# Kernel optimization log

Hardware: AMD Instinct MI355X
Metric: run time of the kernel (lower is better)

Reference implementation:

```python
import jax, jax.numpy as jnp
import numpy as np

N_HEADS = 8
INPUT_DIM = 256
KEY_DIM = 64
VALUE_DIM = 64
BATCH = 16
GRAPH = 1024
NEG_INF = -1e30  # finite stand-in for -inf: safe through softmax under jit/grad


def setup_inputs() -> dict:
    key = jax.random.key(0)
    k_h, k_m, k_q, k_k, k_v = jax.random.split(key, 5)
    h = jax.random.normal(k_h, (BATCH, GRAPH, INPUT_DIM), dtype=jnp.float32)
    # anti-adjacency matrix: 1 = disallowed edge, 0 = allowed
    mask = jax.random.randint(k_m, (GRAPH, GRAPH), 0, 2, dtype=jnp.int32)
    W_Q = jax.random.normal(k_q, (N_HEADS, INPUT_DIM, KEY_DIM), dtype=jnp.float32)
    W_K = jax.random.normal(k_k, (N_HEADS, INPUT_DIM, KEY_DIM), dtype=jnp.float32)
    W_V = jax.random.normal(k_v, (N_HEADS, INPUT_DIM, VALUE_DIM), dtype=jnp.float32)
    return {"h": h, "mask": mask, "W_Q": W_Q, "W_K": W_K, "W_V": W_V}


def reference(h, mask, W_Q, W_K, W_V):
    # h: [b, g, i]; W_*: [h, i, d]
    scale = 1.0 / jnp.sqrt(jnp.asarray(W_Q.shape[-1], h.dtype))
    q = jnp.einsum('bgi,hik->bhgk', h, W_Q)  # [b,h,g,dk]
    k = jnp.einsum('bgi,hik->bhgk', h, W_K)  # [b,h,g,dk]
    v = jnp.einsum('bgi,hiv->bhgv', h, W_V)  # [b,h,g,dv]
    compat = scale * jnp.einsum('bhqk,bhmk->bhqm', q, k)  # [b,h,g,g]
    allowed = (mask == 0)  # [g,g], broadcasts over batch/heads
    compat = jnp.where(allowed, compat, NEG_INF)
    attention = jax.nn.softmax(compat, axis=-1)
    # original zeroes attention at masked positions after softmax
    attention = jnp.where(allowed, attention, 0.0)
    h_p = jnp.einsum('bhqm,bhmv->bhqv', attention, v)  # [b,h,g,dv]
    return h_p
```

## Files before the change

### kernel.cpp

```cpp
#include <hip/hip_runtime.h>
#include <math.h>

typedef __bf16 bf16x8 __attribute__((ext_vector_type(8)));
typedef float  f32x4  __attribute__((ext_vector_type(4)));

#define NEGB   (-1.4426950408889634e30f)
#define SCALE2 (0.18033688011112042f)

template <int N> struct ic { static constexpr int value = N; };

static __device__ __forceinline__ f32x4 mfma16(bf16x8 a, bf16x8 b, f32x4 c) {
    return __builtin_amdgcn_mfma_f32_16x16x32_bf16(a, b, c, 0, 0, 0);
}

static __device__ __forceinline__ void load_lds16(const void* g, void* l) {
    __builtin_amdgcn_global_load_lds(
        (const __attribute__((address_space(1))) unsigned int*)g,
        (__attribute__((address_space(3))) unsigned int*)l, 16, 0, 0);
}

template <int CTRL>
static __device__ __forceinline__ float dppf(float x) {
    int xi = __builtin_bit_cast(int, x);
    int r = __builtin_amdgcn_update_dpp(xi, xi, CTRL, 0xf, 0xf, false);
    return __builtin_bit_cast(float, r);
}
static __device__ __forceinline__ float rowmax16(float x) {
    x = fmaxf(x, dppf<0x128>(x));
    x = fmaxf(x, dppf<0x124>(x));
    x = fmaxf(x, dppf<0x122>(x));
    x = fmaxf(x, dppf<0x121>(x));
    return x;
}
static __device__ __forceinline__ float rowsum16(float x) {
    x += dppf<0x128>(x);
    x += dppf<0x124>(x);
    x += dppf<0x122>(x);
    x += dppf<0x121>(x);
    return x;
}

#define RAW_BARRIER() asm volatile("s_waitcnt lgkmcnt(0)\n\ts_barrier" ::: "memory")

__global__ void prep_kernel(const int* __restrict__ mask,
                            const float* __restrict__ Wq, const float* __restrict__ Wk,
                            const float* __restrict__ Wv,
                            unsigned long long* __restrict__ mbits,
                            __bf16* __restrict__ Whi_t, __bf16* __restrict__ Wlo_t)
{
    const int tid = threadIdx.x;
    if (blockIdx.x < 1024) {
        const int row = blockIdx.x, wave = tid >> 6, lane = tid & 63;
        #pragma unroll
        for (int i = 0; i < 4; ++i) {
            int word = wave * 4 + i;
            int m = mask[row * 1024 + word * 64 + lane];
            unsigned long long b = __ballot(m != 0);
            if (lane == 0) mbits[row * 16 + word] = b;
        }
    } else {
        int idx = (blockIdx.x - 1024) * 256 + tid;
        int lane = idx & 63, t = (idx >> 6) & 3, kc = (idx >> 8) & 7;
        int head = (idx >> 11) & 7, mat = idx >> 14;
        int quad = lane >> 4, ln = lane & 15;
        const float* W = (mat == 0 ? Wq : (mat == 1 ? Wk : Wv)) + head * 16384;
        bf16x8 hi, lo;
        #pragma unroll
        for (int j = 0; j < 8; ++j) {
            float w = W[(kc * 32 + quad * 8 + j) * 64 + t * 16 + ln];
            __bf16 hh = (__bf16)w;
            hi[j] = hh;
            lo[j] = (__bf16)(w - (float)hh);
        }
        *(bf16x8*)(Whi_t + (size_t)idx * 8) = hi;
        *(bf16x8*)(Wlo_t + (size_t)idx * 8) = lo;
    }
}

__global__ __launch_bounds__(256, 2) void projkv_kernel(
    const float* __restrict__ X,
    const __bf16* __restrict__ Whi_t, const __bf16* __restrict__ Wlo_t,
    unsigned char* __restrict__ khi_g, unsigned char* __restrict__ klo_g,
    unsigned char* __restrict__ vT_g)
{
    const int head = blockIdx.x, rt = blockIdx.y;
    const int tid = threadIdx.x, wave = tid >> 6, lane = tid & 63;
    const int quad = lane >> 4, ln = lane & 15;

    __shared__ __align__(16) unsigned char SL[24576];

    const float* xr = X + ((size_t)(rt * 64 + wave * 16 + ln)) * 256;
    bf16x8 ahi[8], alo[8];
    #pragma unroll
    for (int kc = 0; kc < 8; ++kc) {
        f32x4 xa = *(const f32x4*)(xr + kc * 32 + quad * 8);
        f32x4 xb = *(const f32x4*)(xr + kc * 32 + quad * 8 + 4);
        #pragma unroll
        for (int j = 0; j < 4; ++j) {
            __bf16 h0 = (__bf16)xa[j]; ahi[kc][j] = h0; alo[kc][j] = (__bf16)(xa[j] - (float)h0);
            __bf16 h1 = (__bf16)xb[j]; ahi[kc][4 + j] = h1; alo[kc][4 + j] = (__bf16)(xb[j] - (float)h1);
        }
    }

    const __bf16* WhiK = Whi_t + ((size_t)(8 + head) * 2048) * 8;
    const __bf16* WloK = Wlo_t + ((size_t)(8 + head) * 2048) * 8;
    const __bf16* WhiV = Whi_t + ((size_t)(16 + head) * 2048) * 8;

    f32x4 kacc[4], vacc[4];
    #pragma unroll
    for (int t = 0; t < 4; ++t) { kacc[t] = (f32x4){0.f,0.f,0.f,0.f}; vacc[t] = kacc[t]; }

    #pragma unroll
    for (int kc = 0; kc < 8; ++kc) {
        #pragma unroll
        for (int t = 0; t < 4; ++t) {
            size_t fo = (size_t)((kc * 4 + t) * 64 + lane) * 8;
            bf16x8 bhiK = *(const bf16x8*)(WhiK + fo);
            bf16x8 bloK = *(const bf16x8*)(WloK + fo);
            bf16x8 bhiV = *(const bf16x8*)(WhiV + fo);
            kacc[t] = mfma16(ahi[kc], bhiK, kacc[t]);
            kacc[t] = mfma16(alo[kc], bhiK, kacc[t]);
            kacc[t] = mfma16(ahi[kc], bloK, kacc[t]);
            vacc[t] = mfma16(ahi[kc], bhiV, vacc[t]);
        }
    }

    #pragma unroll
    for (int t = 0; t < 4; ++t) {
        #pragma unroll
        for (int r = 0; r < 4; ++r) {
            {
                float val = kacc[t][r];
                __bf16 hh = (__bf16)val;
                __bf16 ll = (__bf16)(val - (float)hh);
                int row = wave * 16 + quad * 4 + r;
                int lc = t * 2 + (ln >> 3);
                int sc = lc ^ (row & 7);
                int off = (row * 8 + sc) * 16 + (ln & 7) * 2;
                *(__bf16*)(SL + off) = hh;
                *(__bf16*)(SL + 8192 + off) = ll;
            }
            {
                int dvrow = t * 16 + ln;
                int m = wave * 16 + quad * 4 + r;
                int lc = m >> 3;
                int sc = lc ^ (ln & 7);
                int off = (dvrow * 8 + sc) * 16 + (m & 7) * 2;
                *(__bf16*)(SL + 16384 + off) = (__bf16)vacc[t][r];
            }
        }
    }
    __syncthreads();

    const int bh = (rt >> 4) * 8 + head;
    const int mt = rt & 15;
    const size_t tb = (size_t)(bh * 16 + mt) * 8192;
    #pragma unroll
    for (int i = 0; i < 2; ++i) {
        int c = (i * 256 + tid) * 16;
        *(uint4*)(khi_g + tb + c) = *(const uint4*)(SL + c);
        *(uint4*)(klo_g + tb + c) = *(const uint4*)(SL + 8192 + c);
        *(uint4*)(vT_g  + tb + c) = *(const uint4*)(SL + 16384 + c);
    }
}

__global__ __launch_bounds__(256, 2) void attn_kernel(
    const float* __restrict__ X,
    const __bf16* __restrict__ Whi_t, const __bf16* __restrict__ Wlo_t,
    const unsigned char* __restrict__ khi_g, const unsigned char* __restrict__ klo_g,
    const unsigned char* __restrict__ vT_g, const unsigned long long* __restrict__ mbits,
    float* __restrict__ out)
{
    const int qt = blockIdx.y;
    const int bh = blockIdx.x;
    const int b = bh >> 3, head = bh & 7;
    const int tid = threadIdx.x, wave = tid >> 6, lane = tid & 63;
    const int quad = lane >> 4, ln = lane & 15;

    __shared__ __align__(16) unsigned char lds[49152];

    f32x4 qacc[2][4];
    #pragma unroll
    for (int rg = 0; rg < 2; ++rg)
        #pragma unroll
        for (int t = 0; t < 4; ++t) qacc[rg][t] = (f32x4){0.f, 0.f, 0.f, 0.f};

    const __bf16* WhiQ = Whi_t + (size_t)head * 2048 * 8;
    const __bf16* WloQ = Wlo_t + (size_t)head * 2048 * 8;

    #pragma unroll
    for (int kc = 0; kc < 8; ++kc) {
        bf16x8 ahi[2], alo[2];
        #pragma unroll
        for (int rg = 0; rg < 2; ++rg) {
            const float* xr = X + ((size_t)b * 1024 + qt * 128 + wave * 32 + rg * 16 + ln) * 256;
            f32x4 xa = *(const f32x4*)(xr + kc * 32 + quad * 8);
            f32x4 xb = *(const f32x4*)(xr + kc * 32 + quad * 8 + 4);
            #pragma unroll
            for (int j = 0; j < 4; ++j) {
                __bf16 h0 = (__bf16)xa[j]; ahi[rg][j] = h0; alo[rg][j] = (__bf16)(xa[j] - (float)h0);
                __bf16 h1 = (__bf16)xb[j]; ahi[rg][4 + j] = h1; alo[rg][4 + j] = (__bf16)(xb[j] - (float)h1);
            }
        }
        #pragma unroll
        for (int t = 0; t < 4; ++t) {
            size_t fo = (size_t)((kc * 4 + t) * 64 + lane) * 8;
            bf16x8 bhi = *(const bf16x8*)(WhiQ + fo);
            bf16x8 blo = *(const bf16x8*)(WloQ + fo);
            #pragma unroll
            for (int rg = 0; rg < 2; ++rg) {
                qacc[rg][t] = mfma16(ahi[rg], bhi, qacc[rg][t]);
                qacc[rg][t] = mfma16(alo[rg], bhi, qacc[rg][t]);
                qacc[rg][t] = mfma16(ahi[rg], blo, qacc[rg][t]);
            }
        }
    }

    #pragma unroll
    for (int rg = 0; rg < 2; ++rg)
        #pragma unroll
        for (int t = 0; t < 4; ++t) {
            qacc[rg][t] *= SCALE2;
            #pragma unroll
            for (int r = 0; r < 4; ++r)
                *(float*)(lds + wave * 8704 + (rg * 16 + quad * 4 + r) * 272 + (t * 16 + ln) * 4) =
                    qacc[rg][t][r];
        }
    bf16x8 qhi[2][2], qlo[2][2];
    #pragma unroll
    for (int rg = 0; rg < 2; ++rg)
        #pragma unroll
        for (int c = 0; c < 2; ++c) {
            f32x4 a0 = *(const f32x4*)(lds + wave * 8704 + (rg * 16 + ln) * 272 + c * 128 + quad * 32);
            f32x4 a1 = *(const f32x4*)(lds + wave * 8704 + (rg * 16 + ln) * 272 + c * 128 + quad * 32 + 16);
            #pragma unroll
            for (int j = 0; j < 4; ++j) {
                __bf16 h0 = (__bf16)a0[j]; qhi[rg][c][j] = h0; qlo[rg][c][j] = (__bf16)(a0[j] - (float)h0);
                __bf16 h1 = (__bf16)a1[j]; qhi[rg][c][4 + j] = h1; qlo[rg][c][4 + j] = (__bf16)(a1[j] - (float)h1);
            }
        }
    __syncthreads();

    int addrA[4][2], addrP[2];
    #pragma unroll
    for (int t = 0; t < 4; ++t)
        #pragma unroll
        for (int c = 0; c < 2; ++c)
            addrA[t][c] = (t * 16 + ln) * 128 + (((c * 4 + quad) ^ (ln & 7)) << 4);
    #pragma unroll
    for (int c = 0; c < 2; ++c)
        addrP[c] = ln * 128 + (((c * 4 + quad) ^ (ln & 7)) << 4);

    f32x4 o[2][4];
    float mrow[2][4], lrow[2][4];
    #pragma unroll
    for (int rg = 0; rg < 2; ++rg)
        #pragma unroll
        for (int t = 0; t < 4; ++t) {
            o[rg][t] = (f32x4){0.f, 0.f, 0.f, 0.f};
            mrow[rg][t] = -INFINITY; lrow[rg][t] = 0.f;
        }

    const int qrow0 = qt * 128 + wave * 32 + quad * 4;

    auto stage = [&](int mt, int bufb) {
        const unsigned char* kb = khi_g + (size_t)(bh * 16 + mt) * 8192;
        const unsigned char* lb = klo_g + (size_t)(bh * 16 + mt) * 8192;
        const unsigned char* vb = vT_g + (size_t)(bh * 16 + mt) * 8192;
        #pragma unroll
        for (int j = 0; j < 2; ++j) {
            int ch = j * 256 + wave * 64;
            load_lds16(kb + (size_t)(ch + lane) * 16, lds + bufb + ch * 16);
            load_lds16(lb + (size_t)(ch + lane) * 16, lds + bufb + 8192 + ch * 16);
            load_lds16(vb + (size_t)(ch + lane) * 16, lds + bufb + 16384 + ch * 16);
        }
    };

    auto step = [&](auto bofc, int mt) {
        constexpr int BOFF = decltype(bofc)::value;
        if (mt < 15) stage(mt + 1, 24576 - BOFF);

        uint2 wm[2][4];
        #pragma unroll
        for (int rg = 0; rg < 2; ++rg)
            #pragma unroll
            for (int r = 0; r < 4; ++r)
                wm[rg][r] = *(const uint2*)((const unsigned char*)mbits +
                                            ((size_t)(qrow0 + rg * 16 + r) * 16 + mt) * 8);

        f32x4 s[2][4];
        #pragma unroll
        for (int rg = 0; rg < 2; ++rg)
            #pragma unroll
            for (int t = 0; t < 4; ++t) s[rg][t] = (f32x4){0.f, 0.f, 0.f, 0.f};
        #pragma unroll
        for (int t = 0; t < 4; ++t)
            #pragma unroll
            for (int c = 0; c < 2; ++c) {
                bf16x8 khi = *(const bf16x8*)(lds + BOFF + addrA[t][c]);
                bf16x8 klo = *(const bf16x8*)(lds + BOFF + 8192 + addrA[t][c]);
                #pragma unroll
                for (int rg = 0; rg < 2; ++rg) {
                    s[rg][t] = mfma16(qhi[rg][c], khi, s[rg][t]);
                    s[rg][t] = mfma16(qlo[rg][c], khi, s[rg][t]);
                    s[rg][t] = mfma16(qhi[rg][c], klo, s[rg][t]);
                }
            }

        RAW_BARRIER();

        #pragma unroll
        for (int rg = 0; rg < 2; ++rg) {
            float pw[4][4], alpha[4];
            #pragma unroll
            for (int r = 0; r < 4; ++r) {
                float sv[4];
                #pragma unroll
                for (int t = 0; t < 4; ++t) {
                    unsigned bits = (t & 2) ? wm[rg][r].y : wm[rg][r].x;
                    float bit = (float)((bits >> ((t & 1) * 16 + ln)) & 1u);
                    sv[t] = fmaf(bit, NEGB, s[rg][t][r]);
                }
                float tm = fmaxf(fmaxf(sv[0], sv[1]), fmaxf(sv[2], sv[3]));
                tm = rowmax16(tm);
                float mn = fmaxf(mrow[rg][r], tm);
                float a = __builtin_amdgcn_exp2f(mrow[rg][r] - mn);
                float rs = 0.f;
                #pragma unroll
                for (int t = 0; t < 4; ++t) {
                    float p = __builtin_amdgcn_exp2f(sv[t] - mn);
                    pw[r][t] = p; rs += p;
                }
                rs = rowsum16(rs);
                lrow[rg][r] = lrow[rg][r] * a + rs;
                mrow[rg][r] = mn;
                alpha[r] = a;
            }
            #pragma unroll
            for (int t = 0; t < 4; ++t)
                #pragma unroll
                for (int r = 0; r < 4; ++r) o[rg][t][r] *= alpha[r];
            #pragma unroll
            for (int t = 0; t < 4; ++t) {
                int lc16 = t * 32 + ((ln >> 3) << 4);
                #pragma unroll
                for (int r = 0; r < 4; ++r) {
                    int row = quad * 4 + r;
                    int addr = BOFF + wave * 4096 + rg * 2048 + row * 128 +
                               (lc16 ^ ((row & 7) << 4)) + ((ln & 7) << 1);
                    *(__bf16*)(lds + addr) = (__bf16)pw[r][t];
                }
            }
        }
        asm volatile("s_waitcnt lgkmcnt(0)" ::: "memory");

        #pragma unroll
        for (int c = 0; c < 2; ++c) {
            bf16x8 pa[2];
            #pragma unroll
            for (int rg = 0; rg < 2; ++rg)
                pa[rg] = *(const bf16x8*)(lds + BOFF + wave * 4096 + rg * 2048 + addrP[c]);
            #pragma unroll
            for (int t = 0; t < 4; ++t) {
                bf16x8 vb = *(const bf16x8*)(lds + BOFF + 16384 + addrA[t][c]);
                #pragma unroll
                for (int rg = 0; rg < 2; ++rg) o[rg][t] = mfma16(pa[rg], vb, o[rg][t]);
            }
        }
        __syncthreads();
    };

    stage(0, 0);
    __syncthreads();
    for (int mp = 0; mp < 8; ++mp) {
        step(ic<0>{}, 2 * mp);
        step(ic<24576>{}, 2 * mp + 1);
    }

    float* ob = out + (size_t)bh * 65536;
    #pragma unroll
    for (int rg = 0; rg < 2; ++rg)
        #pragma unroll
        for (int r = 0; r < 4; ++r) {
            float inv = 1.0f / lrow[rg][r];
            #pragma unroll
            for (int t = 0; t < 4; ++t)
                ob[(size_t)(qrow0 + rg * 16 + r) * 64 + t * 16 + ln] = o[rg][t][r] * inv;
        }
}

extern "C" void kernel_launch(void* const* d_in, const int* in_sizes, int n_in,
                              void* d_out, int out_size, void* d_ws, size_t ws_size,
                              hipStream_t stream) {
    const float* h    = (const float*)d_in[0];
    const int*   mask = (const int*)d_in[1];
    const float* Wq   = (const float*)d_in[2];
    const float* Wk   = (const float*)d_in[3];
    const float* Wv   = (const float*)d_in[4];
    float* out = (float*)d_out;

    unsigned char* ws = (unsigned char*)d_ws;
    unsigned char* khi_g = ws;
    unsigned char* klo_g = ws + 16777216;
    unsigned char* vT_g  = ws + 33554432;
    __bf16* Whi_t = (__bf16*)(ws + 50331648);
    __bf16* Wlo_t = (__bf16*)(ws + 51118080);
    unsigned long long* mbits = (unsigned long long*)(ws + 51904512);

    prep_kernel<<<1216, 256, 0, stream>>>(mask, Wq, Wk, Wv, mbits, Whi_t, Wlo_t);
    projkv_kernel<<<dim3(8, 256), 256, 0, stream>>>(h, Whi_t, Wlo_t, khi_g, klo_g, vT_g);
    attn_kernel<<<dim3(128, 8), 256, 0, stream>>>(h, Whi_t, Wlo_t, khi_g, klo_g, vT_g, mbits, out);
}
```

Measured before the change: 248.4 us.

## Load K/V MFMA fragments directly from global memory and reuse X rows across heads

The attention kernel drops the LDS double-buffered staging of K/V tiles and their block barriers. projkv now writes K and V^T pre-arranged in MFMA fragment order, so each lane reads its bf16x8 operands straight from global memory and only the per-wave P matrix goes through LDS. projkv also handles four heads per block, so X is loaded and split into hi/lo once for four heads instead of once per head. The cost is global/L2 latency exposed inside the inner loop with no explicit prefetch, and fewer, longer projkv blocks.

Measured after the change: 299.9 us. 20.7% more time.

```diff
diff --git a/kernel.cpp b/kernel.cpp
--- a/kernel.cpp
+++ b/kernel.cpp
@@ -7,16 +7,8 @@
 #define NEGB   (-1.4426950408889634e30f)
 #define SCALE2 (0.18033688011112042f)
 
-template <int N> struct ic { static constexpr int value = N; };
-
 static __device__ __forceinline__ f32x4 mfma16(bf16x8 a, bf16x8 b, f32x4 c) {
     return __builtin_amdgcn_mfma_f32_16x16x32_bf16(a, b, c, 0, 0, 0);
-}
-
-static __device__ __forceinline__ void load_lds16(const void* g, void* l) {
-    __builtin_amdgcn_global_load_lds(
-        (const __attribute__((address_space(1))) unsigned int*)g,
-        (__attribute__((address_space(3))) unsigned int*)l, 16, 0, 0);
 }
 
 template <int CTRL>
@@ -39,8 +31,6 @@
     x += dppf<0x121>(x);
     return x;
 }
-
-#define RAW_BARRIER() asm volatile("s_waitcnt lgkmcnt(0)\n\ts_barrier" ::: "memory")
 
 __global__ void prep_kernel(const int* __restrict__ mask,
                             const float* __restrict__ Wq, const float* __restrict__ Wk,
@@ -83,7 +73,8 @@
     unsigned char* __restrict__ khi_g, unsigned char* __restrict__ klo_g,
     unsigned char* __restrict__ vT_g)
 {
-    const int head = blockIdx.x, rt = blockIdx.y;
+    const int hh = blockIdx.x;
+    const int rt = blockIdx.y;
     const int tid = threadIdx.x, wave = tid >> 6, lane = tid & 63;
     const int quad = lane >> 4, ln = lane & 15;
 
@@ -102,65 +93,67 @@
         }
     }
 
-    const __bf16* WhiK = Whi_t + ((size_t)(8 + head) * 2048) * 8;
-    const __bf16* WloK = Wlo_t + ((size_t)(8 + head) * 2048) * 8;
-    const __bf16* WhiV = Whi_t + ((size_t)(16 + head) * 2048) * 8;
-
-    f32x4 kacc[4], vacc[4];
-    #pragma unroll
-    for (int t = 0; t < 4; ++t) { kacc[t] = (f32x4){0.f,0.f,0.f,0.f}; vacc[t] = kacc[t]; }
-
-    #pragma unroll
-    for (int kc = 0; kc < 8; ++kc) {
-        #pragma unroll
-        for (int t = 0; t < 4; ++t) {
-            size_t fo = (size_t)((kc * 4 + t) * 64 + lane) * 8;
-            bf16x8 bhiK = *(const bf16x8*)(WhiK + fo);
-            bf16x8 bloK = *(const bf16x8*)(WloK + fo);
-            bf16x8 bhiV = *(const bf16x8*)(WhiV + fo);
-            kacc[t] = mfma16(ahi[kc], bhiK, kacc[t]);
-            kacc[t] = mfma16(alo[kc], bhiK, kacc[t]);
-            kacc[t] = mfma16(ahi[kc], bloK, kacc[t]);
-            vacc[t] = mfma16(ahi[kc], bhiV, vacc[t]);
-        }
-    }
-
-    #pragma unroll
-    for (int t = 0; t < 4; ++t) {
-        #pragma unroll
-        for (int r = 0; r < 4; ++r) {
-            {
-                float val = kacc[t][r];
-                __bf16 hh = (__bf16)val;
-                __bf16 ll = (__bf16)(val - (float)hh);
-                int row = wave * 16 + quad * 4 + r;
-                int lc = t * 2 + (ln >> 3);
-                int sc = lc ^ (row & 7);
-                int off = (row * 8 + sc) * 16 + (ln & 7) * 2;
-                *(__bf16*)(SL + off) = hh;
-                *(__bf16*)(SL + 8192 + off) = ll;
-            }
-            {
-                int dvrow = t * 16 + ln;
-                int m = wave * 16 + quad * 4 + r;
-                int lc = m >> 3;
-                int sc = lc ^ (ln & 7);
-                int off = (dvrow * 8 + sc) * 16 + (m & 7) * 2;
-                *(__bf16*)(SL + 16384 + off) = (__bf16)vacc[t][r];
-            }
-        }
-    }
-    __syncthreads();
-
-    const int bh = (rt >> 4) * 8 + head;
     const int mt = rt & 15;
-    const size_t tb = (size_t)(bh * 16 + mt) * 8192;
-    #pragma unroll
-    for (int i = 0; i < 2; ++i) {
-        int c = (i * 256 + tid) * 16;
-        *(uint4*)(khi_g + tb + c) = *(const uint4*)(SL + c);
-        *(uint4*)(klo_g + tb + c) = *(const uint4*)(SL + 8192 + c);
-        *(uint4*)(vT_g  + tb + c) = *(const uint4*)(SL + 16384 + c);
+    const int b8 = (rt >> 4) * 8;
+
+    for (int h4 = 0; h4 < 4; ++h4) {
+        const int head = hh * 4 + h4;
+        const __bf16* WhiK = Whi_t + ((size_t)(8 + head) * 2048) * 8;
+        const __bf16* WloK = Wlo_t + ((size_t)(8 + head) * 2048) * 8;
+        const __bf16* WhiV = Whi_t + ((size_t)(16 + head) * 2048) * 8;
+
+        f32x4 kacc[4], vacc[4];
+        #pragma unroll
+        for (int t = 0; t < 4; ++t) { kacc[t] = (f32x4){0.f,0.f,0.f,0.f}; vacc[t] = kacc[t]; }
+
+        #pragma unroll
+        for (int kc = 0; kc < 8; ++kc) {
+            #pragma unroll
+            for (int t = 0; t < 4; ++t) {
+                size_t fo = (size_t)((kc * 4 + t) * 64 + lane) * 8;
+                bf16x8 bhiK = *(const bf16x8*)(WhiK + fo);
+                bf16x8 bloK = *(const bf16x8*)(WloK + fo);
+                bf16x8 bhiV = *(const bf16x8*)(WhiV + fo);
+                kacc[t] = mfma16(ahi[kc], bhiK, kacc[t]);
+                kacc[t] = mfma16(alo[kc], bhiK, kacc[t]);
+                kacc[t] = mfma16(ahi[kc], bloK, kacc[t]);
+                vacc[t] = mfma16(ahi[kc], bhiV, vacc[t]);
+            }
+        }
+
+        #pragma unroll
+        for (int tp = 0; tp < 4; ++tp) {
+            #pragma unroll
+            for (int r = 0; r < 4; ++r) {
+                {
+                    float val = kacc[tp][r];
+                    __bf16 hhv = (__bf16)val;
+                    __bf16 llv = (__bf16)(val - (float)hhv);
+                    int off = ((wave * 2 + (tp >> 1)) * 64 +
+                               ((tp & 1) * 2 + (ln >> 3)) * 16 + quad * 4 + r) * 16 +
+                              (ln & 7) * 2;
+                    *(__bf16*)(SL + off) = hhv;
+                    *(__bf16*)(SL + 8192 + off) = llv;
+                }
+                {
+                    int off = ((tp * 2 + (wave >> 1)) * 64 +
+                               ((wave & 1) * 2 + (quad >> 1)) * 16 + ln) * 16 +
+                              ((quad & 1) * 4 + r) * 2;
+                    *(__bf16*)(SL + 16384 + off) = (__bf16)vacc[tp][r];
+                }
+            }
+        }
+        __syncthreads();
+
+        const size_t tb = (size_t)((b8 + head) * 16 + mt) * 8192;
+        #pragma unroll
+        for (int i = 0; i < 2; ++i) {
+            int c = (i * 256 + tid) * 16;
+            *(uint4*)(khi_g + tb + c) = *(const uint4*)(SL + c);
+            *(uint4*)(klo_g + tb + c) = *(const uint4*)(SL + 8192 + c);
+            *(uint4*)(vT_g  + tb + c) = *(const uint4*)(SL + 16384 + c);
+        }
+        __syncthreads();
     }
 }
 
@@ -177,7 +170,8 @@
     const int tid = threadIdx.x, wave = tid >> 6, lane = tid & 63;
     const int quad = lane >> 4, ln = lane & 15;
 
-    __shared__ __align__(16) unsigned char lds[49152];
+    __shared__ __align__(16) unsigned char lds[34816];
+    unsigned char* wlds = lds + wave * 8704;
 
     f32x4 qacc[2][4];
     #pragma unroll
@@ -223,30 +217,26 @@
             qacc[rg][t] *= SCALE2;
             #pragma unroll
             for (int r = 0; r < 4; ++r)
-                *(float*)(lds + wave * 8704 + (rg * 16 + quad * 4 + r) * 272 + (t * 16 + ln) * 4) =
+                *(float*)(wlds + (rg * 16 + quad * 4 + r) * 272 + (t * 16 + ln) * 4) =
                     qacc[rg][t][r];
         }
+    asm volatile("s_waitcnt lgkmcnt(0)" ::: "memory");
     bf16x8 qhi[2][2], qlo[2][2];
     #pragma unroll
     for (int rg = 0; rg < 2; ++rg)
         #pragma unroll
         for (int c = 0; c < 2; ++c) {
-            f32x4 a0 = *(const f32x4*)(lds + wave * 8704 + (rg * 16 + ln) * 272 + c * 128 + quad * 32);
-            f32x4 a1 = *(const f32x4*)(lds + wave * 8704 + (rg * 16 + ln) * 272 + c * 128 + quad * 32 + 16);
+            f32x4 a0 = *(const f32x4*)(wlds + (rg * 16 + ln) * 272 + c * 128 + quad * 32);
+            f32x4 a1 = *(const f32x4*)(wlds + (rg * 16 + ln) * 272 + c * 128 + quad * 32 + 16);
             #pragma unroll
             for (int j = 0; j < 4; ++j) {
                 __bf16 h0 = (__bf16)a0[j]; qhi[rg][c][j] = h0; qlo[rg][c][j] = (__bf16)(a0[j] - (float)h0);
                 __bf16 h1 = (__bf16)a1[j]; qhi[rg][c][4 + j] = h1; qlo[rg][c][4 + j] = (__bf16)(a1[j] - (float)h1);
             }
         }
-    __syncthreads();
-
-    int addrA[4][2], addrP[2];
-    #pragma unroll
-    for (int t = 0; t < 4; ++t)
-        #pragma unroll
-        for (int c = 0; c < 2; ++c)
-            addrA[t][c] = (t * 16 + ln) * 128 + (((c * 4 + quad) ^ (ln & 7)) << 4);
+    asm volatile("s_waitcnt lgkmcnt(0)" ::: "memory");
+
+    int addrP[2];
     #pragma unroll
     for (int c = 0; c < 2; ++c)
         addrP[c] = ln * 128 + (((c * 4 + quad) ^ (ln & 7)) << 4);
@@ -262,31 +252,21 @@
         }
 
     const int qrow0 = qt * 128 + wave * 32 + quad * 4;
-
-    auto stage = [&](int mt, int bufb) {
-        const unsigned char* kb = khi_g + (size_t)(bh * 16 + mt) * 8192;
-        const unsigned char* lb = klo_g + (size_t)(bh * 16 + mt) * 8192;
-        const unsigned char* vb = vT_g + (size_t)(bh * 16 + mt) * 8192;
-        #pragma unroll
-        for (int j = 0; j < 2; ++j) {
-            int ch = j * 256 + wave * 64;
-            load_lds16(kb + (size_t)(ch + lane) * 16, lds + bufb + ch * 16);
-            load_lds16(lb + (size_t)(ch + lane) * 16, lds + bufb + 8192 + ch * 16);
-            load_lds16(vb + (size_t)(ch + lane) * 16, lds + bufb + 16384 + ch * 16);
-        }
-    };
-
-    auto step = [&](auto bofc, int mt) {
-        constexpr int BOFF = decltype(bofc)::value;
-        if (mt < 15) stage(mt + 1, 24576 - BOFF);
+    const unsigned char* mbase = (const unsigned char*)mbits + (size_t)qrow0 * 128;
+    const int lo16 = lane * 16;
+
+    for (int mt = 0; mt < 16; ++mt) {
+        const size_t tb = (size_t)(bh * 16 + mt) * 8192;
+        const unsigned char* Kh = khi_g + tb;
+        const unsigned char* Kl = klo_g + tb;
+        const unsigned char* Vb = vT_g + tb;
 
         uint2 wm[2][4];
         #pragma unroll
         for (int rg = 0; rg < 2; ++rg)
             #pragma unroll
             for (int r = 0; r < 4; ++r)
-                wm[rg][r] = *(const uint2*)((const unsigned char*)mbits +
-                                            ((size_t)(qrow0 + rg * 16 + r) * 16 + mt) * 8);
+                wm[rg][r] = *(const uint2*)(mbase + rg * 2048 + r * 128 + mt * 8);
 
         f32x4 s[2][4];
         #pragma unroll
@@ -297,8 +277,8 @@
         for (int t = 0; t < 4; ++t)
             #pragma unroll
             for (int c = 0; c < 2; ++c) {
-                bf16x8 khi = *(const bf16x8*)(lds + BOFF + addrA[t][c]);
-                bf16x8 klo = *(const bf16x8*)(lds + BOFF + 8192 + addrA[t][c]);
+                bf16x8 khi = *(const bf16x8*)(Kh + (t * 2 + c) * 1024 + lo16);
+                bf16x8 klo = *(const bf16x8*)(Kl + (t * 2 + c) * 1024 + lo16);
                 #pragma unroll
                 for (int rg = 0; rg < 2; ++rg) {
                     s[rg][t] = mfma16(qhi[rg][c], khi, s[rg][t]);
@@ -307,7 +287,10 @@
                 }
             }
 
-        RAW_BARRIER();
+        bf16x8 vf0[4];
+        #pragma unroll
+        for (int t = 0; t < 4; ++t)
+            vf0[t] = *(const bf16x8*)(Vb + (t * 2) * 1024 + lo16);
 
         #pragma unroll
         for (int rg = 0; rg < 2; ++rg) {
@@ -346,35 +329,31 @@
                 #pragma unroll
                 for (int r = 0; r < 4; ++r) {
                     int row = quad * 4 + r;
-                    int addr = BOFF + wave * 4096 + rg * 2048 + row * 128 +
-                               (lc16 ^ ((row & 7) << 4)) + ((ln & 7) << 1);
-                    *(__bf16*)(lds + addr) = (__bf16)pw[r][t];
+                    int addr = rg * 2048 + row * 128 + (lc16 ^ ((row & 7) << 4)) + ((ln & 7) << 1);
+                    *(__bf16*)(wlds + addr) = (__bf16)pw[r][t];
                 }
             }
         }
         asm volatile("s_waitcnt lgkmcnt(0)" ::: "memory");
+
+        bf16x8 vf1[4];
+        #pragma unroll
+        for (int t = 0; t < 4; ++t)
+            vf1[t] = *(const bf16x8*)(Vb + (t * 2 + 1) * 1024 + lo16);
 
         #pragma unroll
         for (int c = 0; c < 2; ++c) {
             bf16x8 pa[2];
             #pragma unroll
             for (int rg = 0; rg < 2; ++rg)
-                pa[rg] = *(const bf16x8*)(lds + BOFF + wave * 4096 + rg * 2048 + addrP[c]);
+                pa[rg] = *(const bf16x8*)(wlds + rg * 2048 + addrP[c]);
             #pragma unroll
             for (int t = 0; t < 4; ++t) {
-                bf16x8 vb = *(const bf16x8*)(lds + BOFF + 16384 + addrA[t][c]);
+                bf16x8 vb = c ? vf1[t] : vf0[t];
                 #pragma unroll
                 for (int rg = 0; rg < 2; ++rg) o[rg][t] = mfma16(pa[rg], vb, o[rg][t]);
             }
         }
-        __syncthreads();
-    };
-
-    stage(0, 0);
-    __syncthreads();
-    for (int mp = 0; mp < 8; ++mp) {
-        step(ic<0>{}, 2 * mp);
-        step(ic<24576>{}, 2 * mp + 1);
     }
 
     float* ob = out + (size_t)bh * 65536;
@@ -408,6 +387,6 @@
     unsigned long long* mbits = (unsigned long long*)(ws + 51904512);
 
     prep_kernel<<<1216, 256, 0, stream>>>(mask, Wq, Wk, Wv, mbits, Whi_t, Wlo_t);
-    projkv_kernel<<<dim3(8, 256), 256, 0, stream>>>(h, Whi_t, Wlo_t, khi_g, klo_g, vT_g);
+    projkv_kernel<<<dim3(2, 256), 256, 0, stream>>>(h, Whi_t, Wlo_t, khi_g, klo_g, vT_g);
     attn_kernel<<<dim3(128, 8), 256, 0, stream>>>(h, Whi_t, Wlo_t, khi_g, klo_g, vT_g, mbits, out);
 }
```
